# Kernel tuning notes

Hardware: AMD Instinct MI355X
Metric: run time of the kernel (lower is better)

The kernel has to match this reference:

```python
import jax, jax.numpy as jnp
import numpy as np

B, S, H, HS, D = 256, 16, 8, 128, 1024
M = H * HS  # mem_size = 1024
FORGET_BIAS = 1.0


def setup_inputs() -> dict:
    key = jax.random.key(0)
    ks = jax.random.split(key, 16)
    n = lambda k, shape, s=0.02: (jax.random.normal(k, shape, jnp.float32) * s)
    return {
        'inputs': jax.random.normal(ks[0], (B, D), jnp.float32),
        'h_state': jax.random.normal(ks[1], (B, S, M), jnp.float32),
        'm_state': jax.random.normal(ks[2], (B, S, M), jnp.float32),
        'W_emb': n(ks[3], (D, M)), 'b_emb': jnp.zeros((M,), jnp.float32),
        'W_g': n(ks[4], (M, M)), 'b_g': jnp.zeros((M,), jnp.float32),
        'W_wf': n(ks[5], (D, M)), 'W_wi': n(ks[6], (D, M)), 'W_wo': n(ks[7], (D, M)),
        'W_uf': n(ks[8], (M, M)), 'b_uf': jnp.zeros((M,), jnp.float32),
        'W_ui': n(ks[9], (M, M)), 'b_ui': jnp.zeros((M,), jnp.float32),
        'W_uo': n(ks[10], (M, M)), 'b_uo': jnp.zeros((M,), jnp.float32),
    }


def _rmc_forward(inputs, h_state, m_state, W_emb, b_emb, W_g, b_g,
                 W_wf, W_wi, W_wo, W_uf, b_uf, W_ui, b_ui, W_uo, b_uo):
    # input embedding: [B, D] -> [B, M]
    dense_inputs = inputs @ W_emb + b_emb
    # keys/values: memory with the embedded input appended as an extra slot -> [B, S+1, M]
    kv = jnp.concatenate([m_state, dense_inputs[:, None, :]], axis=1)
    # multi-head scaled dot-product attention (no q/k/v projections in AttentionMap)
    q = m_state.reshape(B, S, H, HS)
    k = kv.reshape(B, S + 1, H, HS)
    v = kv.reshape(B, S + 1, H, HS)
    scores = jnp.einsum('bqhd,bkhd->bhqk', q, k) / jnp.sqrt(jnp.asarray(HS, q.dtype))
    attn = jax.nn.softmax(scores, axis=-1)
    attended = jnp.einsum('bhqk,bkhd->bqhd', attn, v).reshape(B, S, M)

    memory_proposal = m_state + attended
    memory_proposal = (memory_proposal @ W_g + b_g) + memory_proposal

    forget_gate = jax.nn.sigmoid(h_state @ W_uf + b_uf + (inputs @ W_wf)[:, None, :])
    input_gate = jax.nn.sigmoid(h_state @ W_ui + b_ui + (inputs @ W_wi)[:, None, :])
    output_gate = jax.nn.sigmoid(h_state @ W_uo + b_uo + (inputs @ W_wo)[:, None, :])

    # NOTE: faithful to the original (including the sigmoid around m*f + bias and
    # the double-sigmoid on the input/output gates)
    new_memories = jax.nn.sigmoid(m_state * forget_gate + FORGET_BIAS) \
        + memory_proposal * jax.nn.sigmoid(input_gate)
    new_hidden = jnp.tanh(m_state) * jax.nn.sigmoid(output_gate)
    return new_memories, new_hidden


def reference(inputs, h_state, m_state, W_emb, b_emb, W_g, b_g,
              W_wf, W_wi, W_wo, W_uf, b_uf, W_ui, b_ui, W_uo, b_uo):
    return _rmc_forward(inputs, h_state, m_state, W_emb, b_emb, W_g, b_g,
                        W_wf, W_wi, W_wo, W_uf, b_uf, W_ui, b_ui, W_uo, b_uo)
```

## Files before the change

### kernel.cpp

```cpp
#include <hip/hip_runtime.h>
#include <hip/hip_bf16.h>


typedef __hip_bfloat16 bf16;
typedef __bf16 bf16x8 __attribute__((ext_vector_type(8)));
typedef float  f32x4  __attribute__((ext_vector_type(4)));
typedef unsigned short u16x8 __attribute__((ext_vector_type(8)));

__device__ __forceinline__ float b2f(bf16 x) { return __bfloat162float(x); }
__device__ __forceinline__ bf16  f2b(float x) { return __float2bfloat16(x); }
__device__ __forceinline__ unsigned short fbits(float x) {
    bf16 b = __float2bfloat16(x);
    return *(unsigned short*)&b;
}
__device__ __forceinline__ float sig(float x) { return 1.0f / (1.0f + __expf(-x)); }
__device__ __forceinline__ float ftanh(float x) {
    return 1.0f - 2.0f / (1.0f + __expf(2.0f * x));
}

__device__ __forceinline__ void gl_lds16(const void* g, void* l) {
    __builtin_amdgcn_global_load_lds(
        (const __attribute__((address_space(1))) void*)g,
        (__attribute__((address_space(3))) void*)l,
        16, 0, 0);
}

__device__ __forceinline__ float4 ld_bf4(const bf16* p) {
    ushort4 u = *(const ushort4*)p;
    float4 r;
    r.x = b2f(*(const bf16*)&u.x);
    r.y = b2f(*(const bf16*)&u.y);
    r.z = b2f(*(const bf16*)&u.z);
    r.w = b2f(*(const bf16*)&u.w);
    return r;
}

__global__ __launch_bounds__(256) void k_prep(
    const float* __restrict__ W_g, const float* __restrict__ W_uf,
    const float* __restrict__ W_ui, const float* __restrict__ W_uo,
    const float* __restrict__ W_emb, const float* __restrict__ W_wf,
    const float* __restrict__ W_wi, const float* __restrict__ W_wo,
    const float* __restrict__ h_state, const float* __restrict__ inputs,
    bf16* __restrict__ wt, bf16* __restrict__ hbf, float* __restrict__ part)
{
    __shared__ __align__(16) char sbuf[32768];
    const int blk = blockIdx.x;
    const int tid = threadIdx.x;

    if (blk < 128) {
        const float* Wsrc4[4] = {W_emb, W_wf, W_wi, W_wo};
        const int ks = blk & 1;
        const int nt = (blk >> 1) & 31;
        const int mt = blk >> 6;
        const int which = nt >> 3;
        const int n0 = (nt & 7) * 128;
        const int m0 = mt * 128;
        const int kbase = ks * 512;
        const float* Wsrc = Wsrc4[which];
        char* LA = sbuf;
        char* LB = sbuf + 16384;

        const int wv = tid >> 6, lane = tid & 63;
        const int mrow = lane & 15, q = lane >> 4;
        const int rb = (wv & 1) * 64, cb = (wv >> 1) * 64;

        const f32x4 zero4 = {0.0f, 0.0f, 0.0f, 0.0f};
        f32x4 acc[4][4];
        #pragma unroll
        for (int i = 0; i < 4; ++i)
            #pragma unroll
            for (int j = 0; j < 4; ++j) acc[i][j] = zero4;

        for (int s = 0; s < 8; ++s) {
            const int k0 = kbase + s * 64;
            #pragma unroll
            for (int r = 0; r < 8; ++r) {
                int lin = r * 256 + tid;
                int row = lin >> 4, f4 = lin & 15;
                float4 v = *(const float4*)(inputs + (size_t)(m0 + row) * 1024 + k0 + f4 * 4);
                ushort4 p;
                p.x = fbits(v.x); p.y = fbits(v.y); p.z = fbits(v.z); p.w = fbits(v.w);
                *(ushort4*)(LA + row * 128 + ((f4 * 8) ^ ((row & 7) << 4))) = p;
            }
            #pragma unroll
            for (int r = 0; r < 2; ++r) {
                int lin = r * 256 + tid;
                int kq = lin >> 5, cq = lin & 31;
                const float* wp = Wsrc + (size_t)(k0 + kq * 4) * 1024 + n0 + cq * 4;
                float4 v0 = *(const float4*)(wp);
                float4 v1 = *(const float4*)(wp + 1024);
                float4 v2 = *(const float4*)(wp + 2048);
                float4 v3 = *(const float4*)(wp + 3072);
                const float* e0 = (const float*)&v0;
                const float* e1 = (const float*)&v1;
                const float* e2 = (const float*)&v2;
                const float* e3 = (const float*)&v3;
                #pragma unroll
                for (int j = 0; j < 4; ++j) {
                    int c = cq * 4 + j;
                    ushort4 p;
                    p.x = fbits(e0[j]); p.y = fbits(e1[j]);
                    p.z = fbits(e2[j]); p.w = fbits(e3[j]);
                    *(ushort4*)(LB + c * 128 + ((kq * 8) ^ ((c & 7) << 4))) = p;
                }
            }
            __syncthreads();
            #pragma unroll
            for (int kk = 0; kk < 2; ++kk) {
                const int kb = kk * 64 + q * 16;
                bf16x8 afr[4], bfr[4];
                #pragma unroll
                for (int i = 0; i < 4; ++i) {
                    int row = rb + i * 16 + mrow;
                    afr[i] = *(const bf16x8*)(LA + row * 128 + (kb ^ ((row & 7) << 4)));
                }
                #pragma unroll
                for (int j = 0; j < 4; ++j) {
                    int n = cb + j * 16 + mrow;
                    bfr[j] = *(const bf16x8*)(LB + n * 128 + (kb ^ ((n & 7) << 4)));
                }
                #pragma unroll
                for (int i = 0; i < 4; ++i)
                    #pragma unroll
                    for (int j = 0; j < 4; ++j)
                        acc[i][j] = __builtin_amdgcn_mfma_f32_16x16x32_bf16(afr[i], bfr[j], acc[i][j], 0, 0, 0);
            }
            __syncthreads();
        }
        float* P = part + ((size_t)(ks * 4 + which) * 256) * 1024;
        #pragma unroll
        for (int j = 0; j < 4; ++j) {
            const int colp = n0 + cb + j * 16 + mrow;
            #pragma unroll
            for (int i = 0; i < 4; ++i)
                #pragma unroll
                for (int r = 0; r < 4; ++r) {
                    const int row = m0 + rb + i * 16 + q * 4 + r;
                    P[(size_t)row * 1024 + colp] = acc[i][j][r];
                }
        }
    } else if (blk < 1152) {
        const float* Ws[4] = {W_g, W_uf, W_ui, W_uo};
        const int t = blk - 128;
        const int plane = t >> 8;
        const int tt = t & 255;
        const int kb = (tt >> 4) * 64;
        const int nb = (tt & 15) * 64;
        const float* W = Ws[plane];
        bf16* Wt = wt + (size_t)plane * (1024 * 1024);
        float (*tl)[65] = (float (*)[65])sbuf;

        #pragma unroll
        for (int it = 0; it < 4; ++it) {
            int lin = it * 256 + tid;
            int kr = lin >> 4, n4 = lin & 15;
            *(float4*)&tl[kr][n4 * 4] =
                *(const float4*)(W + (size_t)(kb + kr) * 1024 + nb + n4 * 4);
        }
        __syncthreads();
        #pragma unroll
        for (int it = 0; it < 2; ++it) {
            int lin = it * 256 + tid;
            int n = lin >> 3, k8 = (lin & 7) * 8;
            u16x8 p;
            #pragma unroll
            for (int j = 0; j < 8; ++j) p[j] = fbits(tl[k8 + j][n]);
            *(u16x8*)(Wt + (size_t)(nb + n) * 1024 + kb + k8) = p;
        }
    } else {
        const int e = blk - 1152;
        size_t idx = ((size_t)e * 256 + tid) * 16;
        #pragma unroll
        for (int hh = 0; hh < 2; ++hh) {
            float4 a = *(const float4*)(h_state + idx + hh * 8);
            float4 b = *(const float4*)(h_state + idx + hh * 8 + 4);
            u16x8 p;
            p[0] = fbits(a.x); p[1] = fbits(a.y); p[2] = fbits(a.z); p[3] = fbits(a.w);
            p[4] = fbits(b.x); p[5] = fbits(b.y); p[6] = fbits(b.z); p[7] = fbits(b.w);
            *(u16x8*)(hbf + idx + hh * 8) = p;
        }
    }
}

__global__ __launch_bounds__(256) void k_attn(
    const float* __restrict__ m_state,
    const float* __restrict__ part,
    const float* __restrict__ b_emb,
    bf16* __restrict__ mp)
{
    const int b = blockIdx.x >> 3;
    const int h = blockIdx.x & 7;
    const int tid = threadIdx.x;

    __shared__ float kv[17][132];
    __shared__ float sc[16][18];

    for (int idx = tid; idx < 17 * 32; idx += 256) {
        int r = idx >> 5, d4 = idx & 31;
        float4 v;
        if (r < 16) {
            v = *(const float4*)&m_state[(size_t)(b * 16 + r) * 1024 + h * 128 + d4 * 4];
        } else {
            float4 v0 = *(const float4*)&part[(size_t)b * 1024 + h * 128 + d4 * 4];
            float4 v1 = *(const float4*)&part[(size_t)(4 * 256 + b) * 1024 + h * 128 + d4 * 4];
            float4 be = *(const float4*)&b_emb[h * 128 + d4 * 4];
            v.x = v0.x + v1.x + be.x;
            v.y = v0.y + v1.y + be.y;
            v.z = v0.z + v1.z + be.z;
            v.w = v0.w + v1.w + be.w;
        }
        *(float4*)&kv[r][d4 * 4] = v;
    }
    __syncthreads();

    for (int p = tid; p < 16 * 17; p += 256) {
        int qi = p / 17, ki = p % 17;
        float dx = 0.f, dy = 0.f, dz = 0.f, dw = 0.f;
        #pragma unroll 8
        for (int d4 = 0; d4 < 32; ++d4) {
            float4 a = *(const float4*)&kv[qi][d4 * 4];
            float4 c = *(const float4*)&kv[ki][d4 * 4];
            dx += a.x * c.x; dy += a.y * c.y; dz += a.z * c.z; dw += a.w * c.w;
        }
        sc[qi][ki] = (dx + dy + dz + dw) * 0.0883883476483184f;
    }
    __syncthreads();

    if (tid < 16) {
        float mx = -1e30f;
        for (int k = 0; k < 17; ++k) mx = fmaxf(mx, sc[tid][k]);
        float s = 0.0f;
        for (int k = 0; k < 17; ++k) { float e = __expf(sc[tid][k] - mx); sc[tid][k] = e; s += e; }
        float inv = 1.0f / s;
        for (int k = 0; k < 17; ++k) sc[tid][k] *= inv;
    }
    __syncthreads();

    for (int p = tid; p < 16 * 32; p += 256) {
        int qi = p >> 5, d4 = p & 31;
        float sx = 0.f, sy = 0.f, sz = 0.f, sw = 0.f;
        #pragma unroll
        for (int k = 0; k < 17; ++k) {
            float w = sc[qi][k];
            float4 v = *(const float4*)&kv[k][d4 * 4];
            sx += w * v.x; sy += w * v.y; sz += w * v.z; sw += w * v.w;
        }
        float4 base = *(const float4*)&kv[qi][d4 * 4];
        size_t off = (size_t)(b * 16 + qi) * 1024 + h * 128 + d4 * 4;
        mp[off + 0] = f2b(base.x + sx);
        mp[off + 1] = f2b(base.y + sy);
        mp[off + 2] = f2b(base.z + sz);
        mp[off + 3] = f2b(base.w + sw);
    }
}

__global__ __launch_bounds__(512, 2) void k_gemm_big(
    const bf16* __restrict__ hbf,
    const bf16* __restrict__ mpb,
    const bf16* __restrict__ wt,
    bf16* __restrict__ pre,
    bf16* __restrict__ preg)
{
    extern __shared__ __align__(16) char smem[];

    int bid = blockIdx.x;
    bid = (bid & 7) * 32 + (bid >> 3);
    const int by = bid & 15;
    const int ct = bid >> 4;
    const int m0 = by * 256;

    const bf16* A; const bf16* Bp; bf16* Cout; int bn0;
    if (ct < 12) {
        A = hbf;
        const int g = ct >> 2;
        bn0 = (ct & 3) * 256;
        Bp = wt + (size_t)(1 + g) * (1024 * 1024);
        Cout = pre + (size_t)g * (4096 * 1024);
    } else {
        A = mpb;
        bn0 = (ct - 12) * 256;
        Bp = wt;
        Cout = preg;
    }

    const int wv = threadIdx.x >> 6;
    const int lane = threadIdx.x & 63;
    const int r8 = lane >> 3, c8 = lane & 7;
    const int mrow = lane & 15, q = lane >> 4;
    const int wr = wv >> 2, wc = wv & 3;

    const f32x4 zero4 = {0.0f, 0.0f, 0.0f, 0.0f};
    f32x4 acc[8][4];
    #pragma unroll
    for (int i = 0; i < 8; ++i)
        #pragma unroll
        for (int j = 0; j < 4; ++j) acc[i][j] = zero4;

    auto STAGE = [&](int buf, int k0) {
        char* sA = smem + buf * 65536;
        char* sB = sA + 32768;
        #pragma unroll
        for (int t = 0; t < 4; ++t) {
            const int rr = wv * 32 + t * 8;
            gl_lds16(A  + (size_t)(m0  + rr + r8) * 1024 + k0 + (c8 ^ r8) * 8, sA + rr * 128);
            gl_lds16(Bp + (size_t)(bn0 + rr + r8) * 1024 + k0 + (c8 ^ r8) * 8, sB + rr * 128);
        }
    };

    STAGE(0, 0);

    #pragma unroll 2
    for (int step = 0; step < 16; ++step) {
        const int cur = step & 1;
        if (step < 15) {
            STAGE(cur ^ 1, (step + 1) * 64);
            asm volatile("s_waitcnt vmcnt(8)" ::: "memory");
        } else {
            asm volatile("s_waitcnt vmcnt(0)" ::: "memory");
        }
        __builtin_amdgcn_s_barrier();
        __builtin_amdgcn_sched_barrier(0);

        const char* sA = smem + cur * 65536;
        const char* sB = sA + 32768;
        #pragma unroll
        for (int kk = 0; kk < 2; ++kk) {
            const int kb = kk * 64 + q * 16;
            bf16x8 afr[8], bfr[4];
            #pragma unroll
            for (int i = 0; i < 8; ++i) {
                const int row = wr * 128 + i * 16 + mrow;
                afr[i] = *(const bf16x8*)(sA + row * 128 + (kb ^ ((row & 7) << 4)));
            }
            #pragma unroll
            for (int j = 0; j < 4; ++j) {
                const int n = wc * 64 + j * 16 + mrow;
                bfr[j] = *(const bf16x8*)(sB + n * 128 + (kb ^ ((n & 7) << 4)));
            }
            #pragma unroll
            for (int i = 0; i < 8; ++i)
                #pragma unroll
                for (int j = 0; j < 4; ++j)
                    acc[i][j] = __builtin_amdgcn_mfma_f32_16x16x32_bf16(afr[i], bfr[j], acc[i][j], 0, 0, 0);
        }
        __builtin_amdgcn_sched_barrier(0);
        __builtin_amdgcn_s_barrier();
    }

    #pragma unroll
    for (int j = 0; j < 4; ++j) {
        const int col = bn0 + wc * 64 + j * 16 + mrow;
        #pragma unroll
        for (int i = 0; i < 8; ++i)
            #pragma unroll
            for (int r = 0; r < 4; ++r) {
                const int row = m0 + wr * 128 + i * 16 + q * 4 + r;
                Cout[(size_t)row * 1024 + col] = f2b(acc[i][j][r]);
            }
    }
}

__global__ __launch_bounds__(256) void k_epi(
    const float* __restrict__ m_state,
    const bf16* __restrict__ mpb,
    const bf16* __restrict__ preg,
    const bf16* __restrict__ pre,
    const float* __restrict__ part,
    const float* __restrict__ b_g, const float* __restrict__ b_uf,
    const float* __restrict__ b_ui, const float* __restrict__ b_uo,
    float* __restrict__ out_mem, float* __restrict__ out_hid)
{
    const int idx = (blockIdx.x * 256 + threadIdx.x) * 4;
    const int row = idx >> 10;
    const int col = idx & 1023;
    const int b = row >> 4;

    float4 m4  = *(const float4*)(m_state + idx);
    float4 mp4 = ld_bf4(mpb + idx);
    float4 pg4 = ld_bf4(preg + idx);
    float4 pf4 = ld_bf4(pre + idx);
    float4 pi4 = ld_bf4(pre + 4194304 + idx);
    float4 po4 = ld_bf4(pre + 8388608 + idx);

    const size_t po = (size_t)b * 1024 + col;
    float4 xfa = *(const float4*)(part + 262144 + po);
    float4 xfb = *(const float4*)(part + 1048576 + 262144 + po);
    float4 xia = *(const float4*)(part + 524288 + po);
    float4 xib = *(const float4*)(part + 1048576 + 524288 + po);
    float4 xoa = *(const float4*)(part + 786432 + po);
    float4 xob = *(const float4*)(part + 1048576 + 786432 + po);
    float4 xf4, xi4, xo4;
    xf4.x = xfa.x + xfb.x; xf4.y = xfa.y + xfb.y; xf4.z = xfa.z + xfb.z; xf4.w = xfa.w + xfb.w;
    xi4.x = xia.x + xib.x; xi4.y = xia.y + xib.y; xi4.z = xia.z + xib.z; xi4.w = xia.w + xib.w;
    xo4.x = xoa.x + xob.x; xo4.y = xoa.y + xob.y; xo4.z = xoa.z + xob.z; xo4.w = xoa.w + xob.w;

    float4 bg4 = *(const float4*)(b_g + col);
    float4 bf4 = *(const float4*)(b_uf + col);
    float4 bi4 = *(const float4*)(b_ui + col);
    float4 bo4 = *(const float4*)(b_uo + col);

    float4 om, oh;
    {
        float mp2 = pg4.x + bg4.x + mp4.x;
        float fg = sig(pf4.x + bf4.x + xf4.x);
        float ig = sig(pi4.x + bi4.x + xi4.x);
        float og = sig(po4.x + bo4.x + xo4.x);
        om.x = sig(m4.x * fg + 1.0f) + mp2 * sig(ig);
        oh.x = ftanh(m4.x) * sig(og);
    }
    {
        float mp2 = pg4.y + bg4.y + mp4.y;
        float fg = sig(pf4.y + bf4.y + xf4.y);
        float ig = sig(pi4.y + bi4.y + xi4.y);
        float og = sig(po4.y + bo4.y + xo4.y);
        om.y = sig(m4.y * fg + 1.0f) + mp2 * sig(ig);
        oh.y = ftanh(m4.y) * sig(og);
    }
    {
        float mp2 = pg4.z + bg4.z + mp4.z;
        float fg = sig(pf4.z + bf4.z + xf4.z);
        float ig = sig(pi4.z + bi4.z + xi4.z);
        float og = sig(po4.z + bo4.z + xo4.z);
        om.z = sig(m4.z * fg + 1.0f) + mp2 * sig(ig);
        oh.z = ftanh(m4.z) * sig(og);
    }
    {
        float mp2 = pg4.w + bg4.w + mp4.w;
        float fg = sig(pf4.w + bf4.w + xf4.w);
        float ig = sig(pi4.w + bi4.w + xi4.w);
        float og = sig(po4.w + bo4.w + xo4.w);
        om.w = sig(m4.w * fg + 1.0f) + mp2 * sig(ig);
        oh.w = ftanh(m4.w) * sig(og);
    }

    *(float4*)(out_mem + idx) = om;
    *(float4*)(out_hid + idx) = oh;
}

extern "C" void kernel_launch(void* const* d_in, const int* in_sizes, int n_in,
                              void* d_out, int out_size, void* d_ws, size_t ws_size,
                              hipStream_t stream)
{
    const float* inputs  = (const float*)d_in[0];
    const float* h_state = (const float*)d_in[1];
    const float* m_state = (const float*)d_in[2];
    const float* W_emb   = (const float*)d_in[3];
    const float* b_emb   = (const float*)d_in[4];
    const float* W_g     = (const float*)d_in[5];
    const float* b_g     = (const float*)d_in[6];
    const float* W_wf    = (const float*)d_in[7];
    const float* W_wi    = (const float*)d_in[8];
    const float* W_wo    = (const float*)d_in[9];
    const float* W_uf    = (const float*)d_in[10];
    const float* b_uf    = (const float*)d_in[11];
    const float* W_ui    = (const float*)d_in[12];
    const float* b_ui    = (const float*)d_in[13];
    const float* W_uo    = (const float*)d_in[14];
    const float* b_uo    = (const float*)d_in[15];

    char* wsb = (char*)d_ws;
    float* part = (float*)wsb;
    bf16*  hbf  = (bf16*)(wsb + 8u  * 1048576u);
    bf16*  mpb  = (bf16*)(wsb + 16u * 1048576u);
    bf16*  wt   = (bf16*)(wsb + 24u * 1048576u);
    bf16*  pre  = (bf16*)(wsb + 32u * 1048576u);
    bf16*  preg = (bf16*)(wsb + 56u * 1048576u);

    float* out_mem = (float*)d_out;
    float* out_hid = out_mem + (size_t)4096 * 1024;

    k_prep<<<dim3(2176), dim3(256), 0, stream>>>(
        W_g, W_uf, W_ui, W_uo, W_emb, W_wf, W_wi, W_wo,
        h_state, inputs, wt, hbf, part);

    k_attn<<<dim3(256 * 8), dim3(256), 0, stream>>>(m_state, part, b_emb, mpb);

    k_gemm_big<<<dim3(256), dim3(512), 131072, stream>>>(hbf, mpb, wt, pre, preg);

    k_epi<<<dim3(4096), dim3(256), 0, stream>>>(
        m_state, mpb, preg, pre, part,
        b_g, b_uf, b_ui, b_uo, out_mem, out_hid);
}
```

Measured before the change: 218.8 us.

## Fuse gate epilogue into GEMM with per-tile four-gate column grouping

Replaces the separate big GEMM and elementwise epilogue kernels with one kernel. Each block computes a 128x64 tile for all four gate matrices (forget, input, output from h_state and the W_g projection from the memory proposal), stages the results in LDS as bf16, and applies the sigmoid/tanh epilogue directly. This removes the write and re-read of four large bf16 pre-activation buffers in global memory and one launch. In exchange the tiles are smaller, with less data reuse per block and lower MFMA intensity, and launch bounds now allow one block per CU.

```diff
diff --git a/kernel.cpp b/kernel.cpp
--- a/kernel.cpp
+++ b/kernel.cpp
@@ -13,6 +13,12 @@
     bf16 b = __float2bfloat16(x);
     return *(unsigned short*)&b;
 }
+__device__ __forceinline__ float bu2f(unsigned short u) {
+    unsigned int x = ((unsigned int)u) << 16;
+    float f;
+    __builtin_memcpy(&f, &x, 4);
+    return f;
+}
 __device__ __forceinline__ float sig(float x) { return 1.0f / (1.0f + __expf(-x)); }
 __device__ __forceinline__ float ftanh(float x) {
     return 1.0f - 2.0f / (1.0f + __expf(2.0f * x));
@@ -23,16 +29,6 @@
         (const __attribute__((address_space(1))) void*)g,
         (__attribute__((address_space(3))) void*)l,
         16, 0, 0);
-}
-
-__device__ __forceinline__ float4 ld_bf4(const bf16* p) {
-    ushort4 u = *(const ushort4*)p;
-    float4 r;
-    r.x = b2f(*(const bf16*)&u.x);
-    r.y = b2f(*(const bf16*)&u.y);
-    r.z = b2f(*(const bf16*)&u.z);
-    r.w = b2f(*(const bf16*)&u.w);
-    return r;
 }
 
 __global__ __launch_bounds__(256) void k_prep(
@@ -254,56 +250,76 @@
     }
 }
 
-__global__ __launch_bounds__(512, 2) void k_gemm_big(
+__device__ __forceinline__ void epi1(
+    float m, float mpv, float f_, float i_, float o_, float g_,
+    float xf, float xi, float xo, float bg, float bfv, float biv, float bov,
+    float& om, float& oh)
+{
+    float mp2 = g_ + bg + mpv;
+    float fg = sig(f_ + bfv + xf);
+    float ig = sig(i_ + biv + xi);
+    float og = sig(o_ + bov + xo);
+    om = sig(m * fg + 1.0f) + mp2 * sig(ig);
+    oh = ftanh(m) * sig(og);
+}
+
+__global__ __launch_bounds__(512, 1) void k_gemm_fused(
     const bf16* __restrict__ hbf,
     const bf16* __restrict__ mpb,
     const bf16* __restrict__ wt,
-    bf16* __restrict__ pre,
-    bf16* __restrict__ preg)
+    const float* __restrict__ m_state,
+    const float* __restrict__ part,
+    const float* __restrict__ b_g, const float* __restrict__ b_uf,
+    const float* __restrict__ b_ui, const float* __restrict__ b_uo,
+    float* __restrict__ out_mem, float* __restrict__ out_hid)
 {
     extern __shared__ __align__(16) char smem[];
 
-    int bid = blockIdx.x;
-    bid = (bid & 7) * 32 + (bid >> 3);
-    const int by = bid & 15;
-    const int ct = bid >> 4;
-    const int m0 = by * 256;
-
-    const bf16* A; const bf16* Bp; bf16* Cout; int bn0;
-    if (ct < 12) {
-        A = hbf;
-        const int g = ct >> 2;
-        bn0 = (ct & 3) * 256;
-        Bp = wt + (size_t)(1 + g) * (1024 * 1024);
-        Cout = pre + (size_t)g * (4096 * 1024);
-    } else {
-        A = mpb;
-        bn0 = (ct - 12) * 256;
-        Bp = wt;
-        Cout = preg;
-    }
+    const int bid = blockIdx.x;
+    const int xcd = bid & 7;
+    const int idx = bid >> 3;
+    const int cx = xcd * 2 + (idx & 1);
+    const int ry = idx >> 1;
+    const int m0 = ry * 128;
+    const int n0 = cx * 64;
 
     const int wv = threadIdx.x >> 6;
     const int lane = threadIdx.x & 63;
     const int r8 = lane >> 3, c8 = lane & 7;
     const int mrow = lane & 15, q = lane >> 4;
-    const int wr = wv >> 2, wc = wv & 3;
+    const int p = wv >> 1;
+    const int rb = (wv & 1) * 64;
+
+    const bf16* wp0 = wt + (size_t)1 * 1048576;
+    const bf16* wp1 = wt + (size_t)2 * 1048576;
+    const bf16* wp2 = wt + (size_t)3 * 1048576;
+    const bf16* wp3 = wt;
 
     const f32x4 zero4 = {0.0f, 0.0f, 0.0f, 0.0f};
-    f32x4 acc[8][4];
+    f32x4 acc[4][4];
     #pragma unroll
-    for (int i = 0; i < 8; ++i)
+    for (int i = 0; i < 4; ++i)
         #pragma unroll
         for (int j = 0; j < 4; ++j) acc[i][j] = zero4;
 
     auto STAGE = [&](int buf, int k0) {
-        char* sA = smem + buf * 65536;
-        char* sB = sA + 32768;
-        #pragma unroll
-        for (int t = 0; t < 4; ++t) {
-            const int rr = wv * 32 + t * 8;
-            gl_lds16(A  + (size_t)(m0  + rr + r8) * 1024 + k0 + (c8 ^ r8) * 8, sA + rr * 128);
-            gl_lds16(Bp + (size_t)(bn0 + rr + r8) * 1024 + k0 + (c8 ^ r8) * 8, sB + rr * 128);
+        char* sH = smem + buf * 65536;
+        char* sM = sH + 16384;
+        char* sB = sH + 32768;
+        #pragma unroll
+        for (int t = 0; t < 2; ++t) {
+            const int rr = wv * 16 + t * 8 + r8;
+            gl_lds16(hbf + (size_t)(m0 + rr) * 1024 + k0 + (c8 ^ r8) * 8,
+                     sH + rr * 128 - r8 * 128 + r8 * 128);
+            gl_lds16(mpb + (size_t)(m0 + rr) * 1024 + k0 + (c8 ^ r8) * 8,
+                     sM + rr * 128 - r8 * 128 + r8 * 128);
+        }
+        {
+            const int cc = wv * 8 + r8;
+            gl_lds16(wp0 + (size_t)(n0 + cc) * 1024 + k0 + (c8 ^ r8) * 8, sB + 0 * 8192 + cc * 128);
+            gl_lds16(wp1 + (size_t)(n0 + cc) * 1024 + k0 + (c8 ^ r8) * 8, sB + 1 * 8192 + cc * 128);
+            gl_lds16(wp2 + (size_t)(n0 + cc) * 1024 + k0 + (c8 ^ r8) * 8, sB + 2 * 8192 + cc * 128);
+            gl_lds16(wp3 + (size_t)(n0 + cc) * 1024 + k0 + (c8 ^ r8) * 8, sB + 3 * 8192 + cc * 128);
         }
     };
 
@@ -321,24 +337,24 @@
         __builtin_amdgcn_s_barrier();
         __builtin_amdgcn_sched_barrier(0);
 
-        const char* sA = smem + cur * 65536;
-        const char* sB = sA + 32768;
+        const char* sA = smem + cur * 65536 + (p == 3 ? 16384 : 0);
+        const char* sBp = smem + cur * 65536 + 32768 + p * 8192;
         #pragma unroll
         for (int kk = 0; kk < 2; ++kk) {
             const int kb = kk * 64 + q * 16;
-            bf16x8 afr[8], bfr[4];
-            #pragma unroll
-            for (int i = 0; i < 8; ++i) {
-                const int row = wr * 128 + i * 16 + mrow;
+            bf16x8 afr[4], bfr[4];
+            #pragma unroll
+            for (int i = 0; i < 4; ++i) {
+                const int row = rb + i * 16 + mrow;
                 afr[i] = *(const bf16x8*)(sA + row * 128 + (kb ^ ((row & 7) << 4)));
             }
             #pragma unroll
             for (int j = 0; j < 4; ++j) {
-                const int n = wc * 64 + j * 16 + mrow;
-                bfr[j] = *(const bf16x8*)(sB + n * 128 + (kb ^ ((n & 7) << 4)));
-            }
-            #pragma unroll
-            for (int i = 0; i < 8; ++i)
+                const int n = j * 16 + mrow;
+                bfr[j] = *(const bf16x8*)(sBp + n * 128 + (kb ^ ((n & 7) << 4)));
+            }
+            #pragma unroll
+            for (int i = 0; i < 4; ++i)
                 #pragma unroll
                 for (int j = 0; j < 4; ++j)
                     acc[i][j] = __builtin_amdgcn_mfma_f32_16x16x32_bf16(afr[i], bfr[j], acc[i][j], 0, 0, 0);
@@ -347,94 +363,74 @@
         __builtin_amdgcn_s_barrier();
     }
 
+    __syncthreads();
+    bf16* sO = (bf16*)smem;
+    const int OS = 72;
+    const int PS = 128 * 72;
     #pragma unroll
-    for (int j = 0; j < 4; ++j) {
-        const int col = bn0 + wc * 64 + j * 16 + mrow;
-        #pragma unroll
-        for (int i = 0; i < 8; ++i)
+    for (int i = 0; i < 4; ++i)
+        #pragma unroll
+        for (int j = 0; j < 4; ++j)
             #pragma unroll
             for (int r = 0; r < 4; ++r) {
-                const int row = m0 + wr * 128 + i * 16 + q * 4 + r;
-                Cout[(size_t)row * 1024 + col] = f2b(acc[i][j][r]);
-            }
-    }
-}
-
-__global__ __launch_bounds__(256) void k_epi(
-    const float* __restrict__ m_state,
-    const bf16* __restrict__ mpb,
-    const bf16* __restrict__ preg,
-    const bf16* __restrict__ pre,
-    const float* __restrict__ part,
-    const float* __restrict__ b_g, const float* __restrict__ b_uf,
-    const float* __restrict__ b_ui, const float* __restrict__ b_uo,
-    float* __restrict__ out_mem, float* __restrict__ out_hid)
-{
-    const int idx = (blockIdx.x * 256 + threadIdx.x) * 4;
-    const int row = idx >> 10;
-    const int col = idx & 1023;
-    const int b = row >> 4;
-
-    float4 m4  = *(const float4*)(m_state + idx);
-    float4 mp4 = ld_bf4(mpb + idx);
-    float4 pg4 = ld_bf4(preg + idx);
-    float4 pf4 = ld_bf4(pre + idx);
-    float4 pi4 = ld_bf4(pre + 4194304 + idx);
-    float4 po4 = ld_bf4(pre + 8388608 + idx);
-
-    const size_t po = (size_t)b * 1024 + col;
-    float4 xfa = *(const float4*)(part + 262144 + po);
-    float4 xfb = *(const float4*)(part + 1048576 + 262144 + po);
-    float4 xia = *(const float4*)(part + 524288 + po);
-    float4 xib = *(const float4*)(part + 1048576 + 524288 + po);
-    float4 xoa = *(const float4*)(part + 786432 + po);
-    float4 xob = *(const float4*)(part + 1048576 + 786432 + po);
-    float4 xf4, xi4, xo4;
-    xf4.x = xfa.x + xfb.x; xf4.y = xfa.y + xfb.y; xf4.z = xfa.z + xfb.z; xf4.w = xfa.w + xfb.w;
-    xi4.x = xia.x + xib.x; xi4.y = xia.y + xib.y; xi4.z = xia.z + xib.z; xi4.w = xia.w + xib.w;
-    xo4.x = xoa.x + xob.x; xo4.y = xoa.y + xob.y; xo4.z = xoa.z + xob.z; xo4.w = xoa.w + xob.w;
-
-    float4 bg4 = *(const float4*)(b_g + col);
-    float4 bf4 = *(const float4*)(b_uf + col);
-    float4 bi4 = *(const float4*)(b_ui + col);
-    float4 bo4 = *(const float4*)(b_uo + col);
-
-    float4 om, oh;
-    {
-        float mp2 = pg4.x + bg4.x + mp4.x;
-        float fg = sig(pf4.x + bf4.x + xf4.x);
-        float ig = sig(pi4.x + bi4.x + xi4.x);
-        float og = sig(po4.x + bo4.x + xo4.x);
-        om.x = sig(m4.x * fg + 1.0f) + mp2 * sig(ig);
-        oh.x = ftanh(m4.x) * sig(og);
-    }
-    {
-        float mp2 = pg4.y + bg4.y + mp4.y;
-        float fg = sig(pf4.y + bf4.y + xf4.y);
-        float ig = sig(pi4.y + bi4.y + xi4.y);
-        float og = sig(po4.y + bo4.y + xo4.y);
-        om.y = sig(m4.y * fg + 1.0f) + mp2 * sig(ig);
-        oh.y = ftanh(m4.y) * sig(og);
-    }
-    {
-        float mp2 = pg4.z + bg4.z + mp4.z;
-        float fg = sig(pf4.z + bf4.z + xf4.z);
-        float ig = sig(pi4.z + bi4.z + xi4.z);
-        float og = sig(po4.z + bo4.z + xo4.z);
-        om.z = sig(m4.z * fg + 1.0f) + mp2 * sig(ig);
-        oh.z = ftanh(m4.z) * sig(og);
-    }
-    {
-        float mp2 = pg4.w + bg4.w + mp4.w;
-        float fg = sig(pf4.w + bf4.w + xf4.w);
-        float ig = sig(pi4.w + bi4.w + xi4.w);
-        float og = sig(po4.w + bo4.w + xo4.w);
-        om.w = sig(m4.w * fg + 1.0f) + mp2 * sig(ig);
-        oh.w = ftanh(m4.w) * sig(og);
-    }
-
-    *(float4*)(out_mem + idx) = om;
-    *(float4*)(out_hid + idx) = oh;
+                const int row = rb + i * 16 + q * 4 + r;
+                const int col = j * 16 + mrow;
+                sO[p * PS + row * OS + col] = f2b(acc[i][j][r]);
+            }
+    __syncthreads();
+
+    const int t = threadIdx.x;
+    const int erow = t >> 2;
+    const int ecol = (t & 3) * 16;
+    const int grow = m0 + erow;
+    const int gcol = n0 + ecol;
+    const int bb = grow >> 4;
+
+    const float* ms  = m_state + (size_t)grow * 1024 + gcol;
+    const bf16*  mpp = mpb + (size_t)grow * 1024 + gcol;
+    const bf16*  sOr = sO + erow * OS + ecol;
+    const float* px  = part + (size_t)bb * 1024 + gcol;
+    float* pom = out_mem + (size_t)grow * 1024 + gcol;
+    float* poh = out_hid + (size_t)grow * 1024 + gcol;
+
+    #pragma unroll
+    for (int u = 0; u < 4; ++u) {
+        float4 m4 = *(const float4*)(ms + u * 4);
+        ushort4 mpu = *(const ushort4*)(mpp + u * 4);
+        ushort4 fu = *(const ushort4*)(sOr + 0 * PS + u * 4);
+        ushort4 iu = *(const ushort4*)(sOr + 1 * PS + u * 4);
+        ushort4 ou = *(const ushort4*)(sOr + 2 * PS + u * 4);
+        ushort4 gu = *(const ushort4*)(sOr + 3 * PS + u * 4);
+
+        float4 xfa = *(const float4*)(px + 1 * 262144 + u * 4);
+        float4 xfb = *(const float4*)(px + 5 * 262144 + u * 4);
+        float4 xia = *(const float4*)(px + 2 * 262144 + u * 4);
+        float4 xib = *(const float4*)(px + 6 * 262144 + u * 4);
+        float4 xoa = *(const float4*)(px + 3 * 262144 + u * 4);
+        float4 xob = *(const float4*)(px + 7 * 262144 + u * 4);
+
+        float4 bg4 = *(const float4*)(b_g  + gcol + u * 4);
+        float4 bf4 = *(const float4*)(b_uf + gcol + u * 4);
+        float4 bi4 = *(const float4*)(b_ui + gcol + u * 4);
+        float4 bo4 = *(const float4*)(b_uo + gcol + u * 4);
+
+        float4 om, oh;
+        epi1(m4.x, bu2f(mpu.x), bu2f(fu.x), bu2f(iu.x), bu2f(ou.x), bu2f(gu.x),
+             xfa.x + xfb.x, xia.x + xib.x, xoa.x + xob.x,
+             bg4.x, bf4.x, bi4.x, bo4.x, om.x, oh.x);
+        epi1(m4.y, bu2f(mpu.y), bu2f(fu.y), bu2f(iu.y), bu2f(ou.y), bu2f(gu.y),
+             xfa.y + xfb.y, xia.y + xib.y, xoa.y + xob.y,
+             bg4.y, bf4.y, bi4.y, bo4.y, om.y, oh.y);
+        epi1(m4.z, bu2f(mpu.z), bu2f(fu.z), bu2f(iu.z), bu2f(ou.z), bu2f(gu.z),
+             xfa.z + xfb.z, xia.z + xib.z, xoa.z + xob.z,
+             bg4.z, bf4.z, bi4.z, bo4.z, om.z, oh.z);
+        epi1(m4.w, bu2f(mpu.w), bu2f(fu.w), bu2f(iu.w), bu2f(ou.w), bu2f(gu.w),
+             xfa.w + xfb.w, xia.w + xib.w, xoa.w + xob.w,
+             bg4.w, bf4.w, bi4.w, bo4.w, om.w, oh.w);
+
+        *(float4*)(pom + u * 4) = om;
+        *(float4*)(poh + u * 4) = oh;
+    }
 }
 
 extern "C" void kernel_launch(void* const* d_in, const int* in_sizes, int n_in,
@@ -463,8 +459,6 @@
     bf16*  hbf  = (bf16*)(wsb + 8u  * 1048576u);
     bf16*  mpb  = (bf16*)(wsb + 16u * 1048576u);
     bf16*  wt   = (bf16*)(wsb + 24u * 1048576u);
-    bf16*  pre  = (bf16*)(wsb + 32u * 1048576u);
-    bf16*  preg = (bf16*)(wsb + 56u * 1048576u);
 
     float* out_mem = (float*)d_out;
     float* out_hid = out_mem + (size_t)4096 * 1024;
@@ -475,9 +469,7 @@
 
     k_attn<<<dim3(256 * 8), dim3(256), 0, stream>>>(m_state, part, b_emb, mpb);
 
-    k_gemm_big<<<dim3(256), dim3(512), 131072, stream>>>(hbf, mpb, wt, pre, preg);
-
-    k_epi<<<dim3(4096), dim3(256), 0, stream>>>(
-        m_state, mpb, preg, pre, part,
+    k_gemm_fused<<<dim3(512), dim3(512), 131072, stream>>>(
+        hbf, mpb, wt, m_state, part,
         b_g, b_uf, b_ui, b_uo, out_mem, out_hid);
 }
```

Result: no change. 221.7 us (+1.3%).
